# Performance work log

Measured on AMD Instinct MI355X. Metric: run time of the kernel, lower is better.

Reference implementation:

```python
import jax, jax.numpy as jnp
import numpy as np

B, H, W, C = 64, 56, 56, 192
HEADS, WS, SHIFT, HID, DEPTH = 6, 7, 3, 768, 2
N = WS * WS
HEAD_DIM = C // HEADS
SCALE = HEAD_DIM ** -0.5


def _rel_index(ws):
    coords = np.stack(np.meshgrid(np.arange(ws), np.arange(ws), indexing='ij'))  # (2,ws,ws)
    cf = coords.reshape(2, -1)
    rel = (cf[:, :, None] - cf[:, None, :]).transpose(1, 2, 0).astype(np.int64)  # (N,N,2)
    rel[:, :, 0] += ws - 1
    rel[:, :, 1] += ws - 1
    rel[:, :, 0] *= 2 * ws - 1
    return rel.sum(-1)  # (N,N) into (2ws-1)^2 table


def _attn_mask(hh, ww, ws, ss):
    img = np.zeros((hh, ww))
    cnt = 0
    for hs in (slice(0, -ws), slice(-ws, -ss), slice(-ss, None)):
        for wsl in (slice(0, -ws), slice(-ws, -ss), slice(-ss, None)):
            img[hs, wsl] = cnt
            cnt += 1
    mw = img.reshape(hh // ws, ws, ww // ws, ws).transpose(0, 2, 1, 3).reshape(-1, ws * ws)
    diff = mw[:, None, :] - mw[:, :, None]  # (nW, N, N)
    return np.where(diff != 0, -100.0, 0.0).astype(np.float32)

REL_IDX = _rel_index(WS)                    # (N,N) static
ATTN_MASK = jnp.asarray(_attn_mask(H, W, WS, SHIFT))  # (nW,N,N) static


def _win_part(x):  # (B,H,W,C) -> (B*nW, N, C)
    b, h, w, c = x.shape
    x = x.reshape(b, h // WS, WS, w // WS, WS, c).transpose(0, 1, 3, 2, 4, 5)
    return x.reshape(-1, N, c)


def _win_rev(wins, h, w):  # (B*nW, N, C) -> (B,H,W,C)
    c = wins.shape[-1]
    b = wins.shape[0] // ((h // WS) * (w // WS))
    x = wins.reshape(b, h // WS, w // WS, WS, WS, c).transpose(0, 1, 3, 2, 4, 5)
    return x.reshape(b, h, w, c)


def _ln(x, g, b):
    mu = x.mean(-1, keepdims=True)
    var = x.var(-1, keepdims=True)
    return (x - mu) * jax.lax.rsqrt(var + 1e-5) * g + b


def setup_inputs() -> dict:
    key = jax.random.key(0)
    ks = jax.random.split(key, 8)
    s = 0.02
    return {
        'x': jax.random.normal(ks[0], (B, H * W, C), jnp.float32),
        'ln1_g': jnp.ones((DEPTH, C), jnp.float32),
        'ln1_b': jnp.zeros((DEPTH, C), jnp.float32),
        'qkv_w': jax.random.normal(ks[1], (DEPTH, C, 3 * C), jnp.float32) * s,
        'qkv_b': jnp.zeros((DEPTH, 3 * C), jnp.float32),
        'rpb': jax.random.normal(ks[2], (DEPTH, (2 * WS - 1) ** 2, HEADS), jnp.float32) * s,
        'proj_w': jax.random.normal(ks[3], (DEPTH, C, C), jnp.float32) * s,
        'proj_b': jnp.zeros((DEPTH, C), jnp.float32),
        'ln2_g': jnp.ones((DEPTH, C), jnp.float32),
        'ln2_b': jnp.zeros((DEPTH, C), jnp.float32),
        'fc1_w': jax.random.normal(ks[4], (DEPTH, C, HID), jnp.float32) * s,
        'fc1_b': jnp.zeros((DEPTH, HID), jnp.float32),
        'fc2_w': jax.random.normal(ks[5], (DEPTH, HID, C), jnp.float32) * s,
        'fc2_b': jnp.zeros((DEPTH, C), jnp.float32),
    }


def _block(x, shift, ln1g, ln1b, qw, qb, rpb_t, pw, pb, ln2g, ln2b, f1w, f1b, f2w, f2b):
    shortcut = x
    h = _ln(x, ln1g, ln1b).reshape(B, H, W, C)
    if shift > 0:
        h = jnp.roll(h, (-shift, -shift), axis=(1, 2))
    xw = _win_part(h)                                   # (B*nW, N, C)
    qkv = xw @ qw + qb                                  # (B*nW, N, 3C)
    qkv = qkv.reshape(-1, N, 3, HEADS, HEAD_DIM)
    q, k, v = qkv[:, :, 0], qkv[:, :, 1], qkv[:, :, 2]  # (B*nW, N, h, d)
    attn = jnp.einsum('wnhd,wmhd->whnm', q * SCALE, k)  # (B*nW, h, N, N)
    bias = rpb_t[REL_IDX.reshape(-1)].reshape(N, N, HEADS).transpose(2, 0, 1)
    attn = attn + bias[None]
    if shift > 0:
        nw = ATTN_MASK.shape[0]
        attn = attn.reshape(B, nw, HEADS, N, N) + ATTN_MASK[None, :, None]
        attn = attn.reshape(-1, HEADS, N, N)
    attn = jax.nn.softmax(attn, axis=-1)
    out = jnp.einsum('whnm,wmhd->wnhd', attn, v).reshape(-1, N, C)
    out = out @ pw + pb
    h = _win_rev(out, H, W)
    if shift > 0:
        h = jnp.roll(h, (shift, shift), axis=(1, 2))
    x = shortcut + h.reshape(B, H * W, C)
    y = _ln(x, ln2g, ln2b)
    y = jax.nn.gelu(y @ f1w + f1b, approximate=False) @ f2w + f2b
    return x + y


def reference(x, ln1_g, ln1_b, qkv_w, qkv_b, rpb, proj_w, proj_b,
              ln2_g, ln2_b, fc1_w, fc1_b, fc2_w, fc2_b):
    for i in range(DEPTH):
        shift = 0 if i % 2 == 0 else SHIFT
        x = _block(x, shift, ln1_g[i], ln1_b[i], qkv_w[i], qkv_b[i], rpb[i],
                   proj_w[i], proj_b[i], ln2_g[i], ln2_b[i],
                   fc1_w[i], fc1_b[i], fc2_w[i], fc2_b[i])
    return x
```

## Files before the change

kernel.cpp:

```cpp
#include <hip/hip_runtime.h>
#include <hip/hip_bf16.h>
#include <math.h>

typedef __attribute__((ext_vector_type(8))) short short8;
typedef __attribute__((ext_vector_type(4))) float floatx4;
typedef __attribute__((ext_vector_type(4))) unsigned short ushort4v;

#define SCALE_F 0.17677669529663689f

__device__ __forceinline__ float bf2f(__hip_bfloat16 v){ return __bfloat162float(v); }

__global__ void wcast_t(const float* __restrict__ src, __hip_bfloat16* __restrict__ dst, int K, int N)
{
    int idx = blockIdx.x * 256 + threadIdx.x;
    if (idx >= K * N) return;
    int n = idx / K, k = idx - n * K;
    dst[idx] = __float2bfloat16(src[(size_t)k * N + n]);
}

__global__ __launch_bounds__(256)
void ln_kernel(const float* __restrict__ x, const float* __restrict__ g,
               const float* __restrict__ bb, __hip_bfloat16* __restrict__ out, int b0)
{
    int wave = threadIdx.x >> 6, lane = threadIdx.x & 63;
    int wr = blockIdx.x * 4 + wave;
    const float* xr = x + ((size_t)b0 * 3136 + wr) * 192;
    float v0 = xr[lane], v1 = xr[lane + 64], v2 = xr[lane + 128];
    float s = v0 + v1 + v2, ss = v0 * v0 + v1 * v1 + v2 * v2;
    #pragma unroll
    for (int o = 32; o; o >>= 1) { s += __shfl_xor(s, o); ss += __shfl_xor(ss, o); }
    float mu = s * (1.f / 192.f);
    float rs = rsqrtf(ss * (1.f / 192.f) - mu * mu + 1e-5f);
    __hip_bfloat16* op = out + (size_t)wr * 192;
    op[lane]       = __float2bfloat16((v0 - mu) * rs * g[lane]       + bb[lane]);
    op[lane + 64]  = __float2bfloat16((v1 - mu) * rs * g[lane + 64]  + bb[lane + 64]);
    op[lane + 128] = __float2bfloat16((v2 - mu) * rs * g[lane + 128] + bb[lane + 128]);
}

__global__ __launch_bounds__(64)
void attn_mfma(const __hip_bfloat16* __restrict__ qkv, const float* __restrict__ rpb,
               __hip_bfloat16* __restrict__ out, int shift)
{
    __shared__ float rp_s[169];
    __shared__ __align__(16) unsigned short Ps[64 * 72];
    const int win = blockIdx.x, head = blockIdx.y;
    const int lane = threadIdx.x;
    const int q = lane >> 4, l = lane & 15;
    const int bl = win >> 6, wrem = win & 63;
    const int wh = wrem >> 3, ww = wrem & 7;
    const __hip_bfloat16* base = qkv + head * 32;

    for (int i = lane; i < 169; i += 64) rp_s[i] = rpb[i * 6 + head];

    auto tokof = [&](int m) -> int {
        int mi = (m * 37) >> 8; int mj = m - mi * 7;
        int hh = wh * 7 + mi + shift; if (hh >= 56) hh -= 56;
        int wp = ww * 7 + mj + shift; if (wp >= 56) wp -= 56;
        return bl * 3136 + hh * 56 + wp;
    };

    short8 kf[4], qf[4];
    #pragma unroll
    for (int t = 0; t < 4; ++t) {
        int m = t * 16 + l; int mc = m < 49 ? m : 48;
        int r = tokof(mc);
        kf[t] = *(const short8*)(base + (size_t)r * 576 + 192 + q * 8);
        qf[t] = *(const short8*)(base + (size_t)r * 576 + q * 8);
    }
    floatx4 st[4][4];
    #pragma unroll
    for (int mt = 0; mt < 4; ++mt)
        #pragma unroll
        for (int nt = 0; nt < 4; ++nt) {
            floatx4 z = {0.f, 0.f, 0.f, 0.f};
            st[mt][nt] = __builtin_amdgcn_mfma_f32_16x16x32_bf16(kf[mt], qf[nt], z, 0, 0, 0);
        }

    short8 vb[2][2];
    #pragma unroll
    for (int mk = 0; mk < 2; ++mk)
        #pragma unroll
        for (int j = 0; j < 8; ++j) {
            int m = mk * 32 + q * 8 + j; int mc = m < 49 ? m : 48;
            int r = tokof(mc);
            const short* vp = (const short*)(base + (size_t)r * 576 + 384 + l);
            vb[mk][0][j] = vp[0];
            vb[mk][1][j] = vp[16];
        }

    const bool edgeH = (wh == 7), edgeW = (ww == 7);
    int mi[16], mj[16], idm[16]; bool mok[16];
    #pragma unroll
    for (int mt = 0; mt < 4; ++mt)
        #pragma unroll
        for (int r = 0; r < 4; ++r) {
            int ii = mt * 4 + r;
            int m = mt * 16 + q * 4 + r;
            int d7 = (m * 37) >> 8;
            mi[ii] = d7; mj[ii] = m - d7 * 7;
            mok[ii] = (m < 49);
            int ih = edgeH ? (d7 < 4 ? 1 : 2) : 0;
            int iw = edgeW ? ((m - d7 * 7) < 4 ? 1 : 2) : 0;
            idm[ii] = ih * 3 + iw;
        }
    __syncthreads();

    #pragma unroll
    for (int nt = 0; nt < 4; ++nt) {
        int n = nt * 16 + l;
        int ri = (n * 37) >> 8; int rj = n - ri * 7;
        int ihn = edgeH ? (ri < 4 ? 1 : 2) : 0;
        int iwn = edgeW ? (rj < 4 ? 1 : 2) : 0;
        int idn = ihn * 3 + iwn;
        float sv[16];
        float mx = -3e38f;
        #pragma unroll
        for (int mt = 0; mt < 4; ++mt)
            #pragma unroll
            for (int r = 0; r < 4; ++r) {
                int ii = mt * 4 + r;
                float s = st[mt][nt][r] * SCALE_F + rp_s[(ri - mi[ii] + 6) * 13 + (rj - mj[ii] + 6)];
                if (shift > 0 && idm[ii] != idn) s -= 100.f;
                if (!mok[ii]) s = -3e38f;
                sv[ii] = s;
                mx = fmaxf(mx, s);
            }
        mx = fmaxf(mx, __shfl_xor(mx, 16));
        mx = fmaxf(mx, __shfl_xor(mx, 32));
        float sum = 0.f;
        #pragma unroll
        for (int ii = 0; ii < 16; ++ii) { float e = __expf(sv[ii] - mx); sv[ii] = e; sum += e; }
        sum += __shfl_xor(sum, 16);
        sum += __shfl_xor(sum, 32);
        float inv = 1.f / sum;
        #pragma unroll
        for (int mt = 0; mt < 4; ++mt) {
            ushort4v pk;
            #pragma unroll
            for (int r = 0; r < 4; ++r) {
                __hip_bfloat16 h = __float2bfloat16(sv[mt * 4 + r] * inv);
                pk[r] = *(unsigned short*)&h;
            }
            *(ushort4v*)(&Ps[(size_t)(nt * 16 + l) * 72 + mt * 16 + q * 4]) = pk;
        }
    }
    __syncthreads();

    floatx4 o[4][2];
    #pragma unroll
    for (int nt = 0; nt < 4; ++nt)
        #pragma unroll
        for (int dt = 0; dt < 2; ++dt) o[nt][dt] = floatx4{0.f, 0.f, 0.f, 0.f};
    #pragma unroll
    for (int mk = 0; mk < 2; ++mk)
        #pragma unroll
        for (int nt = 0; nt < 4; ++nt) {
            short8 pf = *(const short8*)(&Ps[(size_t)(nt * 16 + l) * 72 + mk * 32 + q * 8]);
            #pragma unroll
            for (int dt = 0; dt < 2; ++dt)
                o[nt][dt] = __builtin_amdgcn_mfma_f32_16x16x32_bf16(pf, vb[mk][dt], o[nt][dt], 0, 0, 0);
        }
    #pragma unroll
    for (int nt = 0; nt < 4; ++nt)
        #pragma unroll
        for (int r = 0; r < 4; ++r) {
            int n = nt * 16 + q * 4 + r;
            if (n < 49) {
                int tn = tokof(n);
                __hip_bfloat16* op = out + (size_t)tn * 192 + head * 32 + l;
                op[0]  = __float2bfloat16(o[nt][0][r]);
                op[16] = __float2bfloat16(o[nt][1][r]);
            }
        }
}

#define AST 200

__device__ __forceinline__ void stage_a192(const __hip_bfloat16* Atile, __hip_bfloat16* As, int tid)
{
    #pragma unroll
    for (int i = 0; i < 12; ++i) {
        int c = i * 256 + tid;
        int row = (c * 2731) >> 16;
        int col = c - row * 24;
        uint4 v = *(const uint4*)(Atile + (size_t)c * 8);
        *(uint4*)(As + row * AST + col * 8) = v;
    }
}

__device__ __forceinline__ void stage_b192(const __hip_bfloat16* Btile, __hip_bfloat16* Bs, int tid)
{
    #pragma unroll
    for (int i = 0; i < 6; ++i) {
        int c = i * 256 + tid;
        int row = (c * 2731) >> 16;
        int col = c - row * 24;
        uint4 v = *(const uint4*)(Btile + (size_t)c * 8);
        *(uint4*)(Bs + row * AST + col * 8) = v;
    }
}

__device__ __forceinline__ void stage_b_async(const __hip_bfloat16* __restrict__ Wtile,
                                              void* BsBuf, const int* srcoff, int wave)
{
    const char* src = (const char*)Wtile;
    char* dst = (char*)BsBuf + wave * 6144;
    #pragma unroll
    for (int j = 0; j < 6; ++j) {
        __builtin_amdgcn_global_load_lds(
            (const __attribute__((address_space(1))) void*)(src + srcoff[j]),
            (__attribute__((address_space(3))) void*)(dst + j * 1024),
            16, 0, 0);
    }
}

__device__ __forceinline__ void stage_a_async(const __hip_bfloat16* __restrict__ Atile,
                                              void* smem, const int* asrc, int wave)
{
    const char* src = (const char*)Atile;
    char* dst = (char*)smem + wave * 1024;
    #pragma unroll
    for (int i = 0; i < 12; ++i) {
        __builtin_amdgcn_global_load_lds(
            (const __attribute__((address_space(1))) void*)(src + asrc[i]),
            (__attribute__((address_space(3))) void*)(dst + i * 4096),
            16, 0, 0);
    }
}

template<int EPI, int NT>
__global__ __launch_bounds__(256, 2)
void gemm_k192(const __hip_bfloat16* __restrict__ A,
               const __hip_bfloat16* __restrict__ Wt,
               const float* __restrict__ bias,
               __hip_bfloat16* __restrict__ out, int ld)
{
    __shared__ __align__(16) unsigned short smem[128 * 192];
    const int tid = threadIdx.x;
    const int wave = tid >> 6, lane = tid & 63;
    const int q = lane >> 4, l = lane & 15;
    const int wr = wave >> 1, wc = wave & 1;
    const int row0 = blockIdx.x * 128;

    int asrc[12];
    #pragma unroll
    for (int i = 0; i < 12; ++i) {
        int g = i * 256 + tid;
        int row = (g * 2731) >> 16;
        int col = g - row * 24;
        asrc[i] = row * 384 + ((col ^ (row & 7)) << 4);
    }
    stage_a_async(A + (size_t)row0 * 192, smem, asrc, wave);

    int srcoff[6];
    #pragma unroll
    for (int j = 0; j < 6; ++j) {
        int g = (wave * 6 + j) * 64 + lane;
        int row = (g * 2731) >> 16;
        int col = g - row * 24;
        srcoff[j] = row * 384 + ((col ^ (row & 7)) << 4);
    }

    int xk[6];
    #pragma unroll
    for (int k = 0; k < 6; ++k) xk[k] = ((k * 4 + q) ^ (l & 7)) << 4;

    __syncthreads();

    short8 af[4][6];
    const char* sbase = (const char*)smem;
    #pragma unroll
    for (int rt = 0; rt < 4; ++rt) {
        int rb = (wr * 64 + rt * 16 + l) * 384;
        #pragma unroll
        for (int k = 0; k < 6; ++k)
            af[rt][k] = *(const short8*)(sbase + rb + xk[k]);
    }

    __syncthreads();

    stage_b_async(Wt, smem, srcoff, wave);
    __syncthreads();

    for (int ct = 0; ct < NT; ++ct) {
        if (ct + 1 < NT)
            stage_b_async(Wt + (size_t)(ct + 1) * 64 * 192,
                          (char*)smem + ((ct + 1) & 1) * 24576, srcoff, wave);

        const char* bsb = (const char*)smem + (ct & 1) * 24576;
        floatx4 acc[4][2];
        #pragma unroll
        for (int rt = 0; rt < 4; ++rt)
            #pragma unroll
            for (int c = 0; c < 2; ++c) acc[rt][c] = floatx4{0.f, 0.f, 0.f, 0.f};

        #pragma unroll
        for (int k = 0; k < 6; ++k) {
            #pragma unroll
            for (int c = 0; c < 2; ++c) {
                short8 bf = *(const short8*)(bsb + ((wc * 2 + c) * 16 + l) * 384 + xk[k]);
                #pragma unroll
                for (int rt = 0; rt < 4; ++rt)
                    acc[rt][c] = __builtin_amdgcn_mfma_f32_16x16x32_bf16(af[rt][k], bf, acc[rt][c], 0, 0, 0);
            }
        }

        __syncthreads();

        #pragma unroll
        for (int c = 0; c < 2; ++c) {
            int col = ct * 64 + wc * 32 + c * 16 + l;
            float bz = bias[col];
            #pragma unroll
            for (int rt = 0; rt < 4; ++rt)
                #pragma unroll
                for (int rr = 0; rr < 4; ++rr) {
                    int row = row0 + wr * 64 + rt * 16 + q * 4 + rr;
                    float v = acc[rt][c][rr] + bz;
                    if constexpr (EPI == 1)
                        v = 0.5f * v * (1.f + erff(v * 0.70710678118654752f));
                    out[(size_t)row * ld + col] = __float2bfloat16(v);
                }
        }
    }
}

__global__ __launch_bounds__(256)
void gemm_proj_ln(const __hip_bfloat16* __restrict__ A,
                  const __hip_bfloat16* __restrict__ Wt,
                  const float* __restrict__ pb,
                  const float* __restrict__ g2, const float* __restrict__ b2,
                  const float* __restrict__ resid, float* __restrict__ Rout,
                  __hip_bfloat16* __restrict__ lnout, int b0)
{
    __shared__ __align__(16) __hip_bfloat16 As[128 * AST];
    __shared__ __align__(16) __hip_bfloat16 Bs[64 * AST];
    const int tid = threadIdx.x;
    const int wave = tid >> 6, lane = tid & 63;
    const int q = lane >> 4, l = lane & 15;
    const int row0 = blockIdx.x * 128;

    stage_a192(A + (size_t)row0 * 192, As, tid);

    floatx4 acc[2][12];
    #pragma unroll
    for (int rt = 0; rt < 2; ++rt)
        #pragma unroll
        for (int j = 0; j < 12; ++j) acc[rt][j] = floatx4{0.f, 0.f, 0.f, 0.f};

    for (int ct = 0; ct < 3; ++ct) {
        __syncthreads();
        stage_b192(Wt + (size_t)ct * 64 * 192, Bs, tid);
        __syncthreads();
        #pragma unroll
        for (int k = 0; k < 6; ++k) {
            short8 a0 = *(const short8*)(As + (wave * 32 + l) * AST + k * 32 + q * 8);
            short8 a1 = *(const short8*)(As + (wave * 32 + 16 + l) * AST + k * 32 + q * 8);
            #pragma unroll
            for (int c = 0; c < 4; ++c) {
                short8 bf = *(const short8*)(Bs + (c * 16 + l) * AST + k * 32 + q * 8);
                acc[0][ct * 4 + c] = __builtin_amdgcn_mfma_f32_16x16x32_bf16(a0, bf, acc[0][ct * 4 + c], 0, 0, 0);
                acc[1][ct * 4 + c] = __builtin_amdgcn_mfma_f32_16x16x32_bf16(a1, bf, acc[1][ct * 4 + c], 0, 0, 0);
            }
        }
    }

    float gj[12], bj[12], pbj[12];
    #pragma unroll
    for (int j = 0; j < 12; ++j) {
        int col = (j >> 2) * 64 + (j & 3) * 16 + l;
        gj[j] = g2[col]; bj[j] = b2[col]; pbj[j] = pb[col];
    }
    #pragma unroll
    for (int rt = 0; rt < 2; ++rt)
        #pragma unroll
        for (int rr = 0; rr < 4; ++rr) {
            int row = row0 + wave * 32 + rt * 16 + q * 4 + rr;
            size_t rb = ((size_t)b0 * 3136 + row) * 192;
            float y[12];
            float s = 0.f, ss = 0.f;
            #pragma unroll
            for (int j = 0; j < 12; ++j) {
                int col = (j >> 2) * 64 + (j & 3) * 16 + l;
                float v = acc[rt][j][rr] + pbj[j] + resid[rb + col];
                y[j] = v; s += v; ss += v * v;
                Rout[rb + col] = v;
            }
            s += __shfl_xor(s, 1); ss += __shfl_xor(ss, 1);
            s += __shfl_xor(s, 2); ss += __shfl_xor(ss, 2);
            s += __shfl_xor(s, 4); ss += __shfl_xor(ss, 4);
            s += __shfl_xor(s, 8); ss += __shfl_xor(ss, 8);
            float mu = s * (1.f / 192.f);
            float rs = rsqrtf(ss * (1.f / 192.f) - mu * mu + 1e-5f);
            #pragma unroll
            for (int j = 0; j < 12; ++j) {
                int col = (j >> 2) * 64 + (j & 3) * 16 + l;
                lnout[(size_t)row * 192 + col] = __float2bfloat16((y[j] - mu) * rs * gj[j] + bj[j]);
            }
        }
}

__global__ __launch_bounds__(256)
void gemm_fc2(const __hip_bfloat16* __restrict__ A,
              const __hip_bfloat16* __restrict__ Wt,
              const float* __restrict__ bias,
              const float* __restrict__ resid, float* __restrict__ out, int b0)
{
    __shared__ __align__(16) __hip_bfloat16 As[128 * AST];
    __shared__ __align__(16) __hip_bfloat16 Bs[64 * AST];
    const int tid = threadIdx.x;
    const int wave = tid >> 6, lane = tid & 63;
    const int q = lane >> 4, l = lane & 15;
    const int row0 = blockIdx.x * 128;

    floatx4 acc[2][12];
    #pragma unroll
    for (int rt = 0; rt < 2; ++rt)
        #pragma unroll
        for (int j = 0; j < 12; ++j) acc[rt][j] = floatx4{0.f, 0.f, 0.f, 0.f};

    for (int kc = 0; kc < 4; ++kc) {
        __syncthreads();
        #pragma unroll
        for (int i = 0; i < 12; ++i) {
            int c = i * 256 + tid;
            int row = (c * 2731) >> 16;
            int col = c - row * 24;
            uint4 v = *(const uint4*)(A + (size_t)(row0 + row) * 768 + kc * 192 + col * 8);
            *(uint4*)(As + row * AST + col * 8) = v;
        }
        for (int ct = 0; ct < 3; ++ct) {
            __syncthreads();
            #pragma unroll
            for (int i = 0; i < 6; ++i) {
                int c = i * 256 + tid;
                int row = (c * 2731) >> 16;
                int col = c - row * 24;
                uint4 v = *(const uint4*)(Wt + (size_t)(ct * 64 + row) * 768 + kc * 192 + col * 8);
                *(uint4*)(Bs + row * AST + col * 8) = v;
            }
            __syncthreads();
            #pragma unroll
            for (int k = 0; k < 6; ++k) {
                short8 a0 = *(const short8*)(As + (wave * 32 + l) * AST + k * 32 + q * 8);
                short8 a1 = *(const short8*)(As + (wave * 32 + 16 + l) * AST + k * 32 + q * 8);
                #pragma unroll
                for (int c = 0; c < 4; ++c) {
                    short8 bf = *(const short8*)(Bs + (c * 16 + l) * AST + k * 32 + q * 8);
                    acc[0][ct * 4 + c] = __builtin_amdgcn_mfma_f32_16x16x32_bf16(a0, bf, acc[0][ct * 4 + c], 0, 0, 0);
                    acc[1][ct * 4 + c] = __builtin_amdgcn_mfma_f32_16x16x32_bf16(a1, bf, acc[1][ct * 4 + c], 0, 0, 0);
                }
            }
        }
    }

    float bzj[12];
    #pragma unroll
    for (int j = 0; j < 12; ++j) {
        int col = (j >> 2) * 64 + (j & 3) * 16 + l;
        bzj[j] = bias[col];
    }
    #pragma unroll
    for (int rt = 0; rt < 2; ++rt)
        #pragma unroll
        for (int rr = 0; rr < 4; ++rr) {
            int row = row0 + wave * 32 + rt * 16 + q * 4 + rr;
            size_t rb = ((size_t)b0 * 3136 + row) * 192;
            #pragma unroll
            for (int j = 0; j < 12; ++j) {
                int col = (j >> 2) * 64 + (j & 3) * 16 + l;
                out[rb + col] = resid[rb + col] + acc[rt][j][rr] + bzj[j];
            }
        }
}

extern "C" void kernel_launch(void* const* d_in, const int* in_sizes, int n_in,
                              void* d_out, int out_size, void* d_ws, size_t ws_size,
                              hipStream_t stream)
{
    const float* x      = (const float*)d_in[0];
    const float* ln1_g  = (const float*)d_in[1];
    const float* ln1_b  = (const float*)d_in[2];
    const float* qkv_w  = (const float*)d_in[3];
    const float* qkv_b  = (const float*)d_in[4];
    const float* rpb    = (const float*)d_in[5];
    const float* proj_w = (const float*)d_in[6];
    const float* proj_b = (const float*)d_in[7];
    const float* ln2_g  = (const float*)d_in[8];
    const float* ln2_b  = (const float*)d_in[9];
    const float* fc1_w  = (const float*)d_in[10];
    const float* fc1_b  = (const float*)d_in[11];
    const float* fc2_w  = (const float*)d_in[12];
    const float* fc2_b  = (const float*)d_in[13];

    char* ws = (char*)d_ws;
    const size_t RN = 200704ull;

    int CB = 64;
    auto need = [&](int cb) -> size_t {
        return RN * 192 * 4
             + (size_t)cb * 3136 * (192 + 768 + 192) * 2
             + 884736ull * 2 + 4096;
    };
    while (CB > 2 && need(CB) > ws_size) CB >>= 1;

    float* R = (float*)ws;
    size_t off = RN * 192 * 4;
    __hip_bfloat16* bufA = (__hip_bfloat16*)(ws + off); off += (size_t)CB * 3136 * 192 * 2;
    __hip_bfloat16* bufB = (__hip_bfloat16*)(ws + off); off += (size_t)CB * 3136 * 768 * 2;
    __hip_bfloat16* bufC = (__hip_bfloat16*)(ws + off); off += (size_t)CB * 3136 * 192 * 2;
    __hip_bfloat16* wreg = (__hip_bfloat16*)(ws + off);

    __hip_bfloat16 *qkvWt[2], *projWt[2], *fc1Wt[2], *fc2Wt[2];
    size_t woff = 0;
    for (int d = 0; d < 2; ++d) { qkvWt[d] = wreg + woff; woff += 576 * 192; }
    for (int d = 0; d < 2; ++d) { projWt[d] = wreg + woff; woff += 192 * 192; }
    for (int d = 0; d < 2; ++d) { fc1Wt[d] = wreg + woff; woff += 768 * 192; }
    for (int d = 0; d < 2; ++d) { fc2Wt[d] = wreg + woff; woff += 192 * 768; }

    for (int d = 0; d < 2; ++d) {
        wcast_t<<<(192 * 576 + 255) / 256, 256, 0, stream>>>(qkv_w + (size_t)d * 192 * 576, qkvWt[d], 192, 576);
        wcast_t<<<(192 * 192 + 255) / 256, 256, 0, stream>>>(proj_w + (size_t)d * 192 * 192, projWt[d], 192, 192);
        wcast_t<<<(192 * 768 + 255) / 256, 256, 0, stream>>>(fc1_w + (size_t)d * 192 * 768, fc1Wt[d], 192, 768);
        wcast_t<<<(768 * 192 + 255) / 256, 256, 0, stream>>>(fc2_w + (size_t)d * 768 * 192, fc2Wt[d], 768, 192);
    }

    const int nrows = CB * 3136;
    const int gm = nrows / 128;
    for (int d = 0; d < 2; ++d) {
        int shift = d ? 3 : 0;
        const float* residA = d ? R : x;
        const float* rpbd = rpb + (size_t)d * 169 * 6;
        float* outF = d ? (float*)d_out : R;

        for (int b0 = 0; b0 < 64; b0 += CB) {
            ln_kernel<<<nrows / 4, 256, 0, stream>>>(residA, ln1_g + d * 192, ln1_b + d * 192, bufA, b0);
            gemm_k192<0, 9><<<gm, 256, 0, stream>>>(bufA, qkvWt[d], qkv_b + d * 576, bufB, 576);
            attn_mfma<<<dim3(CB * 64, 6), 64, 0, stream>>>(bufB, rpbd, bufA, shift);
            gemm_proj_ln<<<gm, 256, 0, stream>>>(bufA, projWt[d], proj_b + d * 192,
                                                 ln2_g + d * 192, ln2_b + d * 192,
                                                 residA, R, bufC, b0);
            gemm_k192<1, 12><<<gm, 256, 0, stream>>>(bufC, fc1Wt[d], fc1_b + d * 768, bufB, 768);
            gemm_fc2<<<gm, 256, 0, stream>>>(bufB, fc2Wt[d], fc2_b + d * 192, R, outF, b0);
        }
    }
}
```

Baseline: 1.964 ms.

## Restructure fc2 GEMM with direct-to-LDS double-buffered weight loads and register A

The fc2 GEMM now uses 64-row tiles (twice the grid) with a 2x2 wave layout. A fragments are loaded straight from global memory into registers and prefetched one K-chunk ahead. Weight tiles are streamed into a double-buffered LDS region via global_load_lds, so the next tile's copy overlaps the current MFMAs and one sync per step replaces two. The aim is to hide load latency and raise occupancy (launch bounds 3), in exchange for higher register pressure and redundant A reads from global.

Result: slower. 2.029 ms (+3.4%).

```diff
diff --git a/kernel.cpp b/kernel.cpp
--- a/kernel.cpp
+++ b/kernel.cpp
@@ -400,77 +400,99 @@
         }
 }
 
-__global__ __launch_bounds__(256)
+__device__ __forceinline__ void fc2_stage_b(const __hip_bfloat16* __restrict__ Wt,
+                                            void* bufbase, int ct, int kc,
+                                            int wave, int lane)
+{
+    const char* src = (const char*)Wt + (size_t)(ct * 64 + lane) * 1536 + kc * 192 + wave * 48;
+    char* dst = (char*)bufbase + wave * 3072;
+    #pragma unroll
+    for (int j = 0; j < 3; ++j) {
+        __builtin_amdgcn_global_load_lds(
+            (const __attribute__((address_space(1))) void*)(src + j * 16),
+            (__attribute__((address_space(3))) void*)(dst + j * 1024),
+            16, 0, 0);
+    }
+}
+
+__global__ __launch_bounds__(256, 3)
 void gemm_fc2(const __hip_bfloat16* __restrict__ A,
               const __hip_bfloat16* __restrict__ Wt,
               const float* __restrict__ bias,
               const float* __restrict__ resid, float* __restrict__ out, int b0)
 {
-    __shared__ __align__(16) __hip_bfloat16 As[128 * AST];
-    __shared__ __align__(16) __hip_bfloat16 Bs[64 * AST];
+    __shared__ __align__(16) char Bs[2][12288];
     const int tid = threadIdx.x;
     const int wave = tid >> 6, lane = tid & 63;
     const int q = lane >> 4, l = lane & 15;
-    const int row0 = blockIdx.x * 128;
-
-    floatx4 acc[2][12];
-    #pragma unroll
-    for (int rt = 0; rt < 2; ++rt)
-        #pragma unroll
-        for (int j = 0; j < 12; ++j) acc[rt][j] = floatx4{0.f, 0.f, 0.f, 0.f};
-
-    for (int kc = 0; kc < 4; ++kc) {
-        __syncthreads();
-        #pragma unroll
-        for (int i = 0; i < 12; ++i) {
-            int c = i * 256 + tid;
-            int row = (c * 2731) >> 16;
-            int col = c - row * 24;
-            uint4 v = *(const uint4*)(A + (size_t)(row0 + row) * 768 + kc * 192 + col * 8);
-            *(uint4*)(As + row * AST + col * 8) = v;
-        }
+    const int wr = wave >> 1, wc = wave & 1;
+    const int row0 = blockIdx.x * 64;
+
+    const char* a0 = (const char*)A + ((size_t)(row0 + wr * 32 + l) * 768 + q * 8) * 2;
+    const char* a1 = a0 + 16 * 1536;
+
+    short8 af[2][2][3];
+    #pragma unroll
+    for (int k = 0; k < 3; ++k) {
+        af[0][0][k] = *(const short8*)(a0 + k * 64);
+        af[0][1][k] = *(const short8*)(a1 + k * 64);
+    }
+    fc2_stage_b(Wt, Bs[0], 0, 0, wave, lane);
+
+    floatx4 acc[3][2][2];
+    #pragma unroll
+    for (int ct = 0; ct < 3; ++ct)
+        #pragma unroll
+        for (int rt = 0; rt < 2; ++rt)
+            #pragma unroll
+            for (int c = 0; c < 2; ++c) acc[ct][rt][c] = floatx4{0.f, 0.f, 0.f, 0.f};
+
+    __syncthreads();
+
+    #pragma unroll
+    for (int kc = 0; kc < 8; ++kc) {
+        const int cur = kc & 1, nxt = cur ^ 1;
+        #pragma unroll
         for (int ct = 0; ct < 3; ++ct) {
+            const int t = kc * 3 + ct;
+            if (t + 1 < 24)
+                fc2_stage_b(Wt, Bs[(t + 1) & 1], ct == 2 ? 0 : ct + 1, kc + (ct == 2 ? 1 : 0),
+                            wave, lane);
+            if (kc < 7) {
+                af[nxt][0][ct] = *(const short8*)(a0 + (kc + 1) * 192 + ct * 64);
+                af[nxt][1][ct] = *(const short8*)(a1 + (kc + 1) * 192 + ct * 64);
+            }
+            const char* bsb = Bs[t & 1];
+            #pragma unroll
+            for (int k = 0; k < 3; ++k) {
+                #pragma unroll
+                for (int c = 0; c < 2; ++c) {
+                    short8 bf = *(const short8*)(bsb + k * 4096 + q * 1024
+                                                 + (wc * 32 + c * 16 + l) * 16);
+                    #pragma unroll
+                    for (int rt = 0; rt < 2; ++rt)
+                        acc[ct][rt][c] = __builtin_amdgcn_mfma_f32_16x16x32_bf16(
+                            af[cur][rt][k], bf, acc[ct][rt][c], 0, 0, 0);
+                }
+            }
             __syncthreads();
-            #pragma unroll
-            for (int i = 0; i < 6; ++i) {
-                int c = i * 256 + tid;
-                int row = (c * 2731) >> 16;
-                int col = c - row * 24;
-                uint4 v = *(const uint4*)(Wt + (size_t)(ct * 64 + row) * 768 + kc * 192 + col * 8);
-                *(uint4*)(Bs + row * AST + col * 8) = v;
-            }
-            __syncthreads();
-            #pragma unroll
-            for (int k = 0; k < 6; ++k) {
-                short8 a0 = *(const short8*)(As + (wave * 32 + l) * AST + k * 32 + q * 8);
-                short8 a1 = *(const short8*)(As + (wave * 32 + 16 + l) * AST + k * 32 + q * 8);
+        }
+    }
+
+    #pragma unroll
+    for (int ct = 0; ct < 3; ++ct)
+        #pragma unroll
+        for (int c = 0; c < 2; ++c) {
+            int col = ct * 64 + wc * 32 + c * 16 + l;
+            float bz = bias[col];
+            #pragma unroll
+            for (int rt = 0; rt < 2; ++rt)
                 #pragma unroll
-                for (int c = 0; c < 4; ++c) {
-                    short8 bf = *(const short8*)(Bs + (c * 16 + l) * AST + k * 32 + q * 8);
-                    acc[0][ct * 4 + c] = __builtin_amdgcn_mfma_f32_16x16x32_bf16(a0, bf, acc[0][ct * 4 + c], 0, 0, 0);
-                    acc[1][ct * 4 + c] = __builtin_amdgcn_mfma_f32_16x16x32_bf16(a1, bf, acc[1][ct * 4 + c], 0, 0, 0);
+                for (int rr = 0; rr < 4; ++rr) {
+                    int row = row0 + wr * 32 + rt * 16 + q * 4 + rr;
+                    size_t rb = ((size_t)b0 * 3136 + row) * 192;
+                    out[rb + col] = resid[rb + col] + acc[ct][rt][c][rr] + bz;
                 }
-            }
-        }
-    }
-
-    float bzj[12];
-    #pragma unroll
-    for (int j = 0; j < 12; ++j) {
-        int col = (j >> 2) * 64 + (j & 3) * 16 + l;
-        bzj[j] = bias[col];
-    }
-    #pragma unroll
-    for (int rt = 0; rt < 2; ++rt)
-        #pragma unroll
-        for (int rr = 0; rr < 4; ++rr) {
-            int row = row0 + wave * 32 + rt * 16 + q * 4 + rr;
-            size_t rb = ((size_t)b0 * 3136 + row) * 192;
-            #pragma unroll
-            for (int j = 0; j < 12; ++j) {
-                int col = (j >> 2) * 64 + (j & 3) * 16 + l;
-                out[rb + col] = resid[rb + col] + acc[rt][j][rr] + bzj[j];
-            }
         }
 }
 
@@ -527,6 +549,7 @@
 
     const int nrows = CB * 3136;
     const int gm = nrows / 128;
+    const int gm64 = nrows / 64;
     for (int d = 0; d < 2; ++d) {
         int shift = d ? 3 : 0;
         const float* residA = d ? R : x;
@@ -541,7 +564,7 @@
                                                  ln2_g + d * 192, ln2_b + d * 192,
                                                  residA, R, bufC, b0);
             gemm_k192<1, 12><<<gm, 256, 0, stream>>>(bufC, fc1Wt[d], fc1_b + d * 768, bufB, 768);
-            gemm_fc2<<<gm, 256, 0, stream>>>(bufB, fc2Wt[d], fc2_b + d * 192, R, outF, b0);
-        }
-    }
-}
+            gemm_fc2<<<gm64, 256, 0, stream>>>(bufB, fc2Wt[d], fc2_b + d * 192, R, outF, b0);
+        }
+    }
+}
```

## Async-stage proj GEMM with swizzled shared memory, register A, double-buffered B

Applied to the files above, without the earlier changes.

Reworks the projection+LayerNorm GEMM kernel. The A tile is loaded asynchronously into one XOR-swizzled shared buffer and kept in registers. That buffer is then reused as a double buffer for the weight tiles, so the next tile's load overlaps the current MFMA work. Launch bounds now request two blocks per SM, and shared memory shrinks to one 48KB region. This cuts sync points and bank conflicts, but adds register pressure from the A fragments and depends on stage_a_async/stage_b_async helpers defined elsewhere.

After: 1.819 ms. 1.08x faster.

```diff
diff --git a/kernel.cpp b/kernel.cpp
--- a/kernel.cpp
+++ b/kernel.cpp
@@ -325,7 +325,7 @@
     }
 }
 
-__global__ __launch_bounds__(256)
+__global__ __launch_bounds__(256, 2)
 void gemm_proj_ln(const __hip_bfloat16* __restrict__ A,
                   const __hip_bfloat16* __restrict__ Wt,
                   const float* __restrict__ pb,
@@ -333,14 +333,50 @@
                   const float* __restrict__ resid, float* __restrict__ Rout,
                   __hip_bfloat16* __restrict__ lnout, int b0)
 {
-    __shared__ __align__(16) __hip_bfloat16 As[128 * AST];
-    __shared__ __align__(16) __hip_bfloat16 Bs[64 * AST];
+    __shared__ __align__(16) unsigned short smem[128 * 192];
     const int tid = threadIdx.x;
     const int wave = tid >> 6, lane = tid & 63;
     const int q = lane >> 4, l = lane & 15;
     const int row0 = blockIdx.x * 128;
 
-    stage_a192(A + (size_t)row0 * 192, As, tid);
+    int asrc[12];
+    #pragma unroll
+    for (int i = 0; i < 12; ++i) {
+        int g = i * 256 + tid;
+        int row = (g * 2731) >> 16;
+        int col = g - row * 24;
+        asrc[i] = row * 384 + ((col ^ (row & 7)) << 4);
+    }
+    stage_a_async(A + (size_t)row0 * 192, smem, asrc, wave);
+
+    int srcoff[6];
+    #pragma unroll
+    for (int j = 0; j < 6; ++j) {
+        int g = (wave * 6 + j) * 64 + lane;
+        int row = (g * 2731) >> 16;
+        int col = g - row * 24;
+        srcoff[j] = row * 384 + ((col ^ (row & 7)) << 4);
+    }
+    int xk[6];
+    #pragma unroll
+    for (int k = 0; k < 6; ++k) xk[k] = ((k * 4 + q) ^ (l & 7)) << 4;
+
+    __syncthreads();
+
+    short8 af[2][6];
+    const char* sbase = (const char*)smem;
+    #pragma unroll
+    for (int rt = 0; rt < 2; ++rt) {
+        int rb = (wave * 32 + rt * 16 + l) * 384;
+        #pragma unroll
+        for (int k = 0; k < 6; ++k)
+            af[rt][k] = *(const short8*)(sbase + rb + xk[k]);
+    }
+
+    __syncthreads();
+
+    stage_b_async(Wt, smem, srcoff, wave);
+    __syncthreads();
 
     floatx4 acc[2][12];
     #pragma unroll
@@ -349,20 +385,21 @@
         for (int j = 0; j < 12; ++j) acc[rt][j] = floatx4{0.f, 0.f, 0.f, 0.f};
 
     for (int ct = 0; ct < 3; ++ct) {
+        if (ct + 1 < 3)
+            stage_b_async(Wt + (size_t)(ct + 1) * 64 * 192,
+                          (char*)smem + ((ct + 1) & 1) * 24576, srcoff, wave);
+
+        const char* bsb = (const char*)smem + (ct & 1) * 24576;
+        #pragma unroll
+        for (int k = 0; k < 6; ++k) {
+            #pragma unroll
+            for (int c = 0; c < 4; ++c) {
+                short8 bf = *(const short8*)(bsb + (c * 16 + l) * 384 + xk[k]);
+                acc[0][ct * 4 + c] = __builtin_amdgcn_mfma_f32_16x16x32_bf16(af[0][k], bf, acc[0][ct * 4 + c], 0, 0, 0);
+                acc[1][ct * 4 + c] = __builtin_amdgcn_mfma_f32_16x16x32_bf16(af[1][k], bf, acc[1][ct * 4 + c], 0, 0, 0);
+            }
+        }
         __syncthreads();
-        stage_b192(Wt + (size_t)ct * 64 * 192, Bs, tid);
-        __syncthreads();
-        #pragma unroll
-        for (int k = 0; k < 6; ++k) {
-            short8 a0 = *(const short8*)(As + (wave * 32 + l) * AST + k * 32 + q * 8);
-            short8 a1 = *(const short8*)(As + (wave * 32 + 16 + l) * AST + k * 32 + q * 8);
-            #pragma unroll
-            for (int c = 0; c < 4; ++c) {
-                short8 bf = *(const short8*)(Bs + (c * 16 + l) * AST + k * 32 + q * 8);
-                acc[0][ct * 4 + c] = __builtin_amdgcn_mfma_f32_16x16x32_bf16(a0, bf, acc[0][ct * 4 + c], 0, 0, 0);
-                acc[1][ct * 4 + c] = __builtin_amdgcn_mfma_f32_16x16x32_bf16(a1, bf, acc[1][ct * 4 + c], 0, 0, 0);
-            }
-        }
     }
 
     float gj[12], bj[12], pbj[12];
```
